# Kernel tuning notes

Measured on AMD Instinct MI355X. Metric: run time of the kernel, lower is better.

## Reference

```python
import jax, jax.numpy as jnp
import numpy as np

B = 256        # graphs in batch
N_PER = 512    # nodes per graph (uniform)
D = 256        # in_dim
DEG = 16       # avg degree
RATIO = 0.5


def setup_inputs() -> dict:
    key = jax.random.key(0)
    k1, k2, k3, k4 = jax.random.split(key, 4)
    N = B * N_PER
    e_per = N_PER * DEG
    x = jax.random.normal(k1, (N, D), dtype=jnp.float32)
    # edges confined within each graph (DGL batched-graph structure)
    src = jax.random.randint(k2, (B, e_per), 0, N_PER)
    dst = jax.random.randint(k3, (B, e_per), 0, N_PER)
    offs = jnp.arange(B, dtype=jnp.int32)[:, None] * N_PER
    src = (src + offs).reshape(-1).astype(jnp.int32)
    dst = (dst + offs).reshape(-1).astype(jnp.int32)
    W = jax.random.normal(k4, (D, 1), dtype=jnp.float32) / np.sqrt(D)
    b = jnp.zeros((1,), dtype=jnp.float32)
    num_nodes = jnp.full((B,), N_PER, dtype=jnp.int32)
    return {"x": x, "W": W, "b": b, "src": src, "dst": dst, "num_nodes": num_nodes}


def reference(x, W, b, src, dst, num_nodes):
    N, d = x.shape
    bsz = num_nodes.shape[0]
    n = N // bsz                     # uniform nodes per graph -> static
    k = int(np.ceil(RATIO * n))      # nodes kept per graph (static)

    # ---- GraphConv(in_dim, 1), DGL default norm='both':
    # score = D_in^{-1/2} A D_out^{-1/2} (x W) + b   (W applied first: out_dim < in_dim)
    ones_e = jnp.ones(src.shape, dtype=x.dtype)
    deg_out = jax.ops.segment_sum(ones_e, src, num_segments=N)
    deg_in = jax.ops.segment_sum(ones_e, dst, num_segments=N)
    h = x @ W                                              # [N, 1]
    h = h * jax.lax.rsqrt(jnp.clip(deg_out, 1.0))[:, None]
    agg = jax.ops.segment_sum(h[src], dst, num_segments=N) # [N, 1]
    score = (agg * jax.lax.rsqrt(jnp.clip(deg_in, 1.0))[:, None] + b)[:, 0]  # [N]

    # ---- topk per graph: dense [B, n] buffer is just a reshape (uniform graphs),
    # sort descending + take first k  ==  lax.top_k
    dense = score.reshape(bsz, n)
    _, idx = jax.lax.top_k(dense, k)                       # [B, k] descending
    perm = (idx + jnp.arange(bsz)[:, None] * n).reshape(-1)  # global node ids [B*k]

    # ---- gather + scale: feature[perm] * tanh(score[perm])
    feat = x[perm] * jnp.tanh(score[perm])[:, None]        # [B*k, D]

    # ---- node_subgraph: edges whose both endpoints survive
    keep = jnp.zeros((N,), dtype=bool).at[perm].set(True)
    edge_mask = keep[src] & keep[dst]                      # [E]
    next_num_nodes = jnp.full((bsz,), k, dtype=jnp.int32)
    return feat, perm, edge_mask, next_num_nodes
```

## Files before the change

kernel.cpp:

```cpp
#include <hip/hip_runtime.h>
#include <math.h>

#define BB    256
#define NPER  512
#define DD    256
#define KK    256
#define EPG   (NPER * 16)
#define NN    (BB * NPER)
#define EE    (BB * EPG)

__global__ __launch_bounds__(512) void k_fused(
        const float* __restrict__ x, const float* __restrict__ W,
        const float* __restrict__ b,
        const int* __restrict__ src, const int* __restrict__ dst,
        float* __restrict__ feat, float* __restrict__ out_perm,
        float* __restrict__ emask, float* __restrict__ nnn) {
    __shared__ unsigned short esrc[EPG];
    __shared__ unsigned short edst[EPG];
    __shared__ int   degs[NPER];
    __shared__ int   degd[NPER];
    __shared__ float hl[NPER];
    __shared__ float aggl[NPER];
    __shared__ float scl[NPER];
    __shared__ unsigned long long keys[NPER];
    __shared__ int   keep[NPER];
    __shared__ int   sel[KK];

    const int g    = blockIdx.x;
    const int t    = threadIdx.x;
    const int wave = t >> 6;
    const int lane = t & 63;

    degs[t] = 0; degd[t] = 0; aggl[t] = 0.0f; keep[t] = 0;
    __syncthreads();

    const int  nbase = g << 9;
    const int4* s4 = (const int4*)(src + (size_t)g * EPG);
    const int4* d4 = (const int4*)(dst + (size_t)g * EPG);
    for (int i = t; i < EPG / 4; i += 512) {
        int4 sv = s4[i], dv = d4[i];
        int e = i * 4;
        unsigned short s0 = (unsigned short)(sv.x - nbase);
        unsigned short s1 = (unsigned short)(sv.y - nbase);
        unsigned short s2 = (unsigned short)(sv.z - nbase);
        unsigned short s3 = (unsigned short)(sv.w - nbase);
        esrc[e] = s0; esrc[e + 1] = s1; esrc[e + 2] = s2; esrc[e + 3] = s3;
        atomicAdd(&degs[s0], 1); atomicAdd(&degs[s1], 1);
        atomicAdd(&degs[s2], 1); atomicAdd(&degs[s3], 1);
        unsigned short t0 = (unsigned short)(dv.x - nbase);
        unsigned short t1 = (unsigned short)(dv.y - nbase);
        unsigned short t2 = (unsigned short)(dv.z - nbase);
        unsigned short t3 = (unsigned short)(dv.w - nbase);
        edst[e] = t0; edst[e + 1] = t1; edst[e + 2] = t2; edst[e + 3] = t3;
        atomicAdd(&degd[t0], 1); atomicAdd(&degd[t1], 1);
        atomicAdd(&degd[t2], 1); atomicAdd(&degd[t3], 1);
    }
    __syncthreads();

    const float4* w4 = (const float4*)W;
    const float4  wv = w4[lane];
    const int rbase = wave * 64;
    for (int it = 0; it < 64; it += 4) {
        const int r0 = rbase + it;
        const float4* p = (const float4*)(x + ((size_t)(nbase + r0) << 8));
        float4 a0 = p[lane];
        float4 a1 = p[64 + lane];
        float4 a2 = p[128 + lane];
        float4 a3 = p[192 + lane];
        float d0 = a0.x * wv.x + a0.y * wv.y + a0.z * wv.z + a0.w * wv.w;
        float d1 = a1.x * wv.x + a1.y * wv.y + a1.z * wv.z + a1.w * wv.w;
        float d2 = a2.x * wv.x + a2.y * wv.y + a2.z * wv.z + a2.w * wv.w;
        float d3 = a3.x * wv.x + a3.y * wv.y + a3.z * wv.z + a3.w * wv.w;
        #pragma unroll
        for (int off = 32; off > 0; off >>= 1) {
            d0 += __shfl_down(d0, off, 64);
            d1 += __shfl_down(d1, off, 64);
            d2 += __shfl_down(d2, off, 64);
            d3 += __shfl_down(d3, off, 64);
        }
        if (lane == 0) {
            hl[r0]     = d0 * rsqrtf(fmaxf((float)degs[r0], 1.0f));
            hl[r0 + 1] = d1 * rsqrtf(fmaxf((float)degs[r0 + 1], 1.0f));
            hl[r0 + 2] = d2 * rsqrtf(fmaxf((float)degs[r0 + 2], 1.0f));
            hl[r0 + 3] = d3 * rsqrtf(fmaxf((float)degs[r0 + 3], 1.0f));
        }
    }
    __syncthreads();

    for (int e = t; e < EPG; e += 512)
        atomicAdd(&aggl[edst[e]], hl[esrc[e]]);
    __syncthreads();

    const float bias = b[0];
    scl[t] = aggl[t] * rsqrtf(fmaxf((float)degd[t], 1.0f)) + bias;
    __syncthreads();

    {
        unsigned int u = __float_as_uint(scl[t]);
        u = (u & 0x80000000u) ? ~u : (u | 0x80000000u);
        keys[t] = ((unsigned long long)u << 32) |
                  (unsigned long long)(0xFFFFFFFFu - (unsigned)t);
    }
    __syncthreads();
    for (int kk = 2; kk <= NPER; kk <<= 1) {
        for (int j = kk >> 1; j > 0; j >>= 1) {
            int i = t, ixj = t ^ j;
            if (ixj > i) {
                unsigned long long a = keys[i], c = keys[ixj];
                bool up = ((i & kk) == 0);
                if (up ? (a < c) : (a > c)) { keys[i] = c; keys[ixj] = a; }
            }
            __syncthreads();
        }
    }
    if (t < KK) {
        unsigned long long kv = keys[t];
        int idx = (int)(0xFFFFFFFFu - (unsigned int)(kv & 0xFFFFFFFFull));
        sel[t] = idx;
        keep[idx] = 1;
        out_perm[(g << 8) + t] = (float)(nbase + idx);
    }
    __syncthreads();

    for (int it = 0; it < 32; it += 2) {
        const int j0 = wave * 32 + it, j1 = j0 + 1;
        const int l0 = sel[j0], l1 = sel[j1];
        const float s0 = tanhf(scl[l0]);
        const float s1 = tanhf(scl[l1]);
        const float4* q0 = (const float4*)(x + ((size_t)(nbase + l0) << 8));
        const float4* q1 = (const float4*)(x + ((size_t)(nbase + l1) << 8));
        float4 v0 = q0[lane], v1 = q1[lane];
        float4 o0 = make_float4(v0.x * s0, v0.y * s0, v0.z * s0, v0.w * s0);
        float4 o1 = make_float4(v1.x * s1, v1.y * s1, v1.z * s1, v1.w * s1);
        ((float4*)(feat + ((size_t)((g << 8) + j0) << 8)))[lane] = o0;
        ((float4*)(feat + ((size_t)((g << 8) + j1) << 8)))[lane] = o1;
    }

    float4* em4 = (float4*)(emask + ((size_t)g << 13));
    for (int i = t; i < EPG / 4; i += 512) {
        int e = i * 4;
        float4 m;
        m.x = (keep[esrc[e]]     & keep[edst[e]])     ? 1.0f : 0.0f;
        m.y = (keep[esrc[e + 1]] & keep[edst[e + 1]]) ? 1.0f : 0.0f;
        m.z = (keep[esrc[e + 2]] & keep[edst[e + 2]]) ? 1.0f : 0.0f;
        m.w = (keep[esrc[e + 3]] & keep[edst[e + 3]]) ? 1.0f : 0.0f;
        em4[i] = m;
    }
    if (g == 0 && t < BB) nnn[t] = (float)KK;
}

extern "C" void kernel_launch(void* const* d_in, const int* in_sizes, int n_in,
                              void* d_out, int out_size, void* d_ws, size_t ws_size,
                              hipStream_t stream) {
    const float* x   = (const float*)d_in[0];
    const float* W   = (const float*)d_in[1];
    const float* b   = (const float*)d_in[2];
    const int*   src = (const int*)d_in[3];
    const int*   dst = (const int*)d_in[4];

    float* out   = (float*)d_out;
    float* feat  = out;
    float* operm = feat + (size_t)BB * KK * DD;
    float* emask = operm + (size_t)BB * KK;
    float* nnn   = emask + (size_t)EE;

    k_fused<<<BB, 512, 0, stream>>>(x, W, b, src, dst, feat, operm, emask, nnn);
}
```

Before: 258.5 us.

## Split fused per-graph kernel into dot, graph-topk, and feature/mask kernels

Splits the single per-graph kernel, which had only 256 blocks, into three launches. A wide grid computes the x·W dot products. A per-graph kernel handles degrees, aggregation and the bitonic top-k. A third wide-grid kernel does the feature gather-scale and the edge mask through a global keep array. The aim is to spread the bandwidth-heavy x reads and feat/mask writes across many more blocks than the original 256. The cost is extra launches, a workspace round trip, and src/dst being read again in the mask kernel.

```diff
diff --git a/kernel.cpp b/kernel.cpp
--- a/kernel.cpp
+++ b/kernel.cpp
@@ -9,12 +9,42 @@
 #define NN    (BB * NPER)
 #define EE    (BB * EPG)
 
-__global__ __launch_bounds__(512) void k_fused(
-        const float* __restrict__ x, const float* __restrict__ W,
-        const float* __restrict__ b,
+__global__ __launch_bounds__(256) void k_dot(const float* __restrict__ x,
+                                             const float* __restrict__ W,
+                                             float* __restrict__ hraw) {
+    const int wave = threadIdx.x >> 6;
+    const int lane = threadIdx.x & 63;
+    const int r0   = blockIdx.x * 16 + wave * 4;
+    const float4 wv = ((const float4*)W)[lane];
+    const float4* p = (const float4*)(x + ((size_t)r0 << 8));
+    float4 a0 = p[lane];
+    float4 a1 = p[64 + lane];
+    float4 a2 = p[128 + lane];
+    float4 a3 = p[192 + lane];
+    float d0 = a0.x * wv.x + a0.y * wv.y + a0.z * wv.z + a0.w * wv.w;
+    float d1 = a1.x * wv.x + a1.y * wv.y + a1.z * wv.z + a1.w * wv.w;
+    float d2 = a2.x * wv.x + a2.y * wv.y + a2.z * wv.z + a2.w * wv.w;
+    float d3 = a3.x * wv.x + a3.y * wv.y + a3.z * wv.z + a3.w * wv.w;
+    #pragma unroll
+    for (int off = 32; off > 0; off >>= 1) {
+        d0 += __shfl_down(d0, off, 64);
+        d1 += __shfl_down(d1, off, 64);
+        d2 += __shfl_down(d2, off, 64);
+        d3 += __shfl_down(d3, off, 64);
+    }
+    if (lane == 0) {
+        hraw[r0]     = d0;
+        hraw[r0 + 1] = d1;
+        hraw[r0 + 2] = d2;
+        hraw[r0 + 3] = d3;
+    }
+}
+
+__global__ __launch_bounds__(512) void k_graph(
+        const float* __restrict__ hraw, const float* __restrict__ b,
         const int* __restrict__ src, const int* __restrict__ dst,
-        float* __restrict__ feat, float* __restrict__ out_perm,
-        float* __restrict__ emask, float* __restrict__ nnn) {
+        int* __restrict__ perm_i, float* __restrict__ tscore,
+        int* __restrict__ keepg, float* __restrict__ out_perm) {
     __shared__ unsigned short esrc[EPG];
     __shared__ unsigned short edst[EPG];
     __shared__ int   degs[NPER];
@@ -24,17 +54,14 @@
     __shared__ float scl[NPER];
     __shared__ unsigned long long keys[NPER];
     __shared__ int   keep[NPER];
-    __shared__ int   sel[KK];
 
-    const int g    = blockIdx.x;
-    const int t    = threadIdx.x;
-    const int wave = t >> 6;
-    const int lane = t & 63;
+    const int g = blockIdx.x;
+    const int t = threadIdx.x;
+    const int nbase = g << 9;
 
     degs[t] = 0; degd[t] = 0; aggl[t] = 0.0f; keep[t] = 0;
     __syncthreads();
 
-    const int  nbase = g << 9;
     const int4* s4 = (const int4*)(src + (size_t)g * EPG);
     const int4* d4 = (const int4*)(dst + (size_t)g * EPG);
     for (int i = t; i < EPG / 4; i += 512) {
@@ -57,42 +84,14 @@
     }
     __syncthreads();
 
-    const float4* w4 = (const float4*)W;
-    const float4  wv = w4[lane];
-    const int rbase = wave * 64;
-    for (int it = 0; it < 64; it += 4) {
-        const int r0 = rbase + it;
-        const float4* p = (const float4*)(x + ((size_t)(nbase + r0) << 8));
-        float4 a0 = p[lane];
-        float4 a1 = p[64 + lane];
-        float4 a2 = p[128 + lane];
-        float4 a3 = p[192 + lane];
-        float d0 = a0.x * wv.x + a0.y * wv.y + a0.z * wv.z + a0.w * wv.w;
-        float d1 = a1.x * wv.x + a1.y * wv.y + a1.z * wv.z + a1.w * wv.w;
-        float d2 = a2.x * wv.x + a2.y * wv.y + a2.z * wv.z + a2.w * wv.w;
-        float d3 = a3.x * wv.x + a3.y * wv.y + a3.z * wv.z + a3.w * wv.w;
-        #pragma unroll
-        for (int off = 32; off > 0; off >>= 1) {
-            d0 += __shfl_down(d0, off, 64);
-            d1 += __shfl_down(d1, off, 64);
-            d2 += __shfl_down(d2, off, 64);
-            d3 += __shfl_down(d3, off, 64);
-        }
-        if (lane == 0) {
-            hl[r0]     = d0 * rsqrtf(fmaxf((float)degs[r0], 1.0f));
-            hl[r0 + 1] = d1 * rsqrtf(fmaxf((float)degs[r0 + 1], 1.0f));
-            hl[r0 + 2] = d2 * rsqrtf(fmaxf((float)degs[r0 + 2], 1.0f));
-            hl[r0 + 3] = d3 * rsqrtf(fmaxf((float)degs[r0 + 3], 1.0f));
-        }
-    }
+    hl[t] = hraw[nbase + t] * rsqrtf(fmaxf((float)degs[t], 1.0f));
     __syncthreads();
 
     for (int e = t; e < EPG; e += 512)
         atomicAdd(&aggl[edst[e]], hl[esrc[e]]);
     __syncthreads();
 
-    const float bias = b[0];
-    scl[t] = aggl[t] * rsqrtf(fmaxf((float)degd[t], 1.0f)) + bias;
+    scl[t] = aggl[t] * rsqrtf(fmaxf((float)degd[t], 1.0f)) + b[0];
     __syncthreads();
 
     {
@@ -116,37 +115,47 @@
     if (t < KK) {
         unsigned long long kv = keys[t];
         int idx = (int)(0xFFFFFFFFu - (unsigned int)(kv & 0xFFFFFFFFull));
-        sel[t] = idx;
-        keep[idx] = 1;
-        out_perm[(g << 8) + t] = (float)(nbase + idx);
+        int r = (g << 8) + t;
+        perm_i[r]   = nbase + idx;
+        out_perm[r] = (float)(nbase + idx);
+        tscore[r]   = tanhf(scl[idx]);
+        keep[idx]   = 1;
     }
     __syncthreads();
+    keepg[nbase + t] = keep[t];
+}
 
-    for (int it = 0; it < 32; it += 2) {
-        const int j0 = wave * 32 + it, j1 = j0 + 1;
-        const int l0 = sel[j0], l1 = sel[j1];
-        const float s0 = tanhf(scl[l0]);
-        const float s1 = tanhf(scl[l1]);
-        const float4* q0 = (const float4*)(x + ((size_t)(nbase + l0) << 8));
-        const float4* q1 = (const float4*)(x + ((size_t)(nbase + l1) << 8));
-        float4 v0 = q0[lane], v1 = q1[lane];
-        float4 o0 = make_float4(v0.x * s0, v0.y * s0, v0.z * s0, v0.w * s0);
-        float4 o1 = make_float4(v1.x * s1, v1.y * s1, v1.z * s1, v1.w * s1);
-        ((float4*)(feat + ((size_t)((g << 8) + j0) << 8)))[lane] = o0;
-        ((float4*)(feat + ((size_t)((g << 8) + j1) << 8)))[lane] = o1;
+#define FEATBLK (BB * KK / 4)
+#define MASKBLK (EE / 4 / 256)
+__global__ __launch_bounds__(256) void k_featmask(
+        const float* __restrict__ x,
+        const int* __restrict__ perm_i, const float* __restrict__ tscore,
+        const int* __restrict__ src, const int* __restrict__ dst,
+        const int* __restrict__ keepg,
+        float* __restrict__ feat, float* __restrict__ emask,
+        float* __restrict__ nnn) {
+    if (blockIdx.x < FEATBLK) {
+        const int wave = threadIdx.x >> 6;
+        const int lane = threadIdx.x & 63;
+        const int r = blockIdx.x * 4 + wave;
+        const int gid = perm_i[r];
+        const float ts = tscore[r];
+        float4 v = ((const float4*)(x + ((size_t)gid << 8)))[lane];
+        float4 o = make_float4(v.x * ts, v.y * ts, v.z * ts, v.w * ts);
+        ((float4*)(feat + ((size_t)r << 8)))[lane] = o;
+    } else {
+        const int mb = blockIdx.x - FEATBLK;
+        const int i = mb * 256 + threadIdx.x;
+        int4 sv = ((const int4*)src)[i];
+        int4 dv = ((const int4*)dst)[i];
+        float4 m;
+        m.x = (keepg[sv.x] & keepg[dv.x]) ? 1.0f : 0.0f;
+        m.y = (keepg[sv.y] & keepg[dv.y]) ? 1.0f : 0.0f;
+        m.z = (keepg[sv.z] & keepg[dv.z]) ? 1.0f : 0.0f;
+        m.w = (keepg[sv.w] & keepg[dv.w]) ? 1.0f : 0.0f;
+        ((float4*)emask)[i] = m;
+        if (mb == 0 && threadIdx.x < BB) nnn[threadIdx.x] = (float)KK;
     }
-
-    float4* em4 = (float4*)(emask + ((size_t)g << 13));
-    for (int i = t; i < EPG / 4; i += 512) {
-        int e = i * 4;
-        float4 m;
-        m.x = (keep[esrc[e]]     & keep[edst[e]])     ? 1.0f : 0.0f;
-        m.y = (keep[esrc[e + 1]] & keep[edst[e + 1]]) ? 1.0f : 0.0f;
-        m.z = (keep[esrc[e + 2]] & keep[edst[e + 2]]) ? 1.0f : 0.0f;
-        m.w = (keep[esrc[e + 3]] & keep[edst[e + 3]]) ? 1.0f : 0.0f;
-        em4[i] = m;
-    }
-    if (g == 0 && t < BB) nnn[t] = (float)KK;
 }
 
 extern "C" void kernel_launch(void* const* d_in, const int* in_sizes, int n_in,
@@ -164,5 +173,13 @@
     float* emask = operm + (size_t)BB * KK;
     float* nnn   = emask + (size_t)EE;
 
-    k_fused<<<BB, 512, 0, stream>>>(x, W, b, src, dst, feat, operm, emask, nnn);
+    float* hraw   = (float*)d_ws;
+    int*   perm_i = (int*)(hraw + NN);
+    float* tscore = (float*)(perm_i + BB * KK);
+    int*   keepg  = (int*)(tscore + BB * KK);
+
+    k_dot     <<<NN / 16, 256, 0, stream>>>(x, W, hraw);
+    k_graph   <<<BB, 512, 0, stream>>>(hraw, b, src, dst, perm_i, tscore, keepg, operm);
+    k_featmask<<<FEATBLK + MASKBLK, 256, 0, stream>>>(x, perm_i, tscore, src, dst,
+                                                      keepg, feat, emask, nnn);
 }
```

New measurement: 261.7 us. Within noise of the previous version (+1.3%).
